# Performance work log

Hardware: AMD Instinct MI355X
Metric: run time of the kernel (lower is better)

Reference implementation:

```python
import jax, jax.numpy as jnp
import numpy as np
import math

B, C, H, W = 4, 128, 180, 180
CCAM, HEADS, DH, N = 256, 4, 32, 20000
HD = HEADS * DH
GAMMA = 0.08
EPS = 1e-6


def setup_inputs() -> dict:
    key = jax.random.key(0)
    ks = jax.random.split(key, 10)
    return {
        "lidar_bev": jax.random.normal(ks[0], (B, C, H, W), jnp.float32),
        "cam_bev_tokens": jax.random.normal(ks[1], (B, N, CCAM), jnp.float32),
        "gate_weights": jax.random.uniform(ks[2], (B, N), jnp.float32),
        "range_alpha": jax.random.uniform(ks[3], (1, 1, H, W), jnp.float32),
        # q_proj: Conv2d(C, HD, 1) -> weight [HD, C] (1x1 conv == per-pixel linear), bias [HD]
        "q_w": jax.random.normal(ks[4], (HD, C), jnp.float32) * 0.02,
        "q_bias": jax.random.normal(ks[5], (HD,), jnp.float32) * 0.02,
        # k/v_proj: Linear(CCAM, HD, bias=False)
        "k_w": jax.random.normal(ks[6], (HD, CCAM), jnp.float32) * 0.02,
        "v_w": jax.random.normal(ks[7], (HD, CCAM), jnp.float32) * 0.02,
        # out: Conv2d(HD, C, 1, bias=False) -> W_out [C, HD]
        "out_w": jax.random.normal(ks[8], (C, HD), jnp.float32) * 0.02,
        "cam_bev_indices": jax.random.randint(ks[9], (B, N, 2), 0, H, jnp.int32),
    }


def reference(lidar_bev, cam_bev_tokens, gate_weights, range_alpha,
              q_w, q_bias, k_w, v_w, out_w, cam_bev_indices):
    scale = 1.0 / math.sqrt(DH)
    # 1x1 conv q projection -> [B, h, d, H*W]
    q = jnp.einsum('bchw,oc->bohw', lidar_bev, q_w) + q_bias[None, :, None, None]
    q = q.reshape(B, HEADS, DH, H * W)

    i = jnp.clip(cam_bev_indices[..., 0], 0, H - 1)
    j = jnp.clip(cam_bev_indices[..., 1], 0, W - 1)
    lin = i * W + j  # [B, N]

    # gather q at sparse BEV locations -> [B, h, d, N]
    q_g = jnp.take_along_axis(q, lin[:, None, None, :], axis=3)

    # k/v projections -> [B, h, d, N]
    k = jnp.einsum('bnc,oc->bno', cam_bev_tokens, k_w).reshape(B, N, HEADS, DH).transpose(0, 2, 3, 1)
    v = jnp.einsum('bnc,oc->bno', cam_bev_tokens, v_w).reshape(B, N, HEADS, DH).transpose(0, 2, 3, 1)

    # elementwise-multiply attention: logits [B, h, N], softmax over the N tokens
    attn = jax.nn.softmax((q_g * k).sum(axis=2) * scale, axis=-1) * gate_weights[:, None, :]
    fused = (attn[:, :, None, :] * v).reshape(B, HD, N)  # [B, h*d, N]
    out_tok = jnp.einsum('co,bon->bcn', out_w, fused)    # [B, C, N]

    # per-batch scatter (index_add) + hit counts (bincount)
    def scatter_b(tok, lin_b):
        df = jnp.zeros((C, H * W), tok.dtype).at[:, lin_b].add(tok)
        hits = jnp.zeros((H * W,), tok.dtype).at[lin_b].add(1.0)
        return df, hits

    delta_flat, hits = jax.vmap(scatter_b)(out_tok, lin)  # [B,C,HW], [B,HW]
    mask = (hits > 0).astype(lidar_bev.dtype)  # [B, HW]

    # mean over hit locations (per batch, per channel), subtract on hits only
    mean_on = (delta_flat * mask[:, None, :]).sum(axis=-1, keepdims=True) \
              / (mask.sum(axis=-1)[:, None, None] + EPS)  # [B, C, 1]
    tmp = (delta_flat - mean_on * mask[:, None, :]).reshape(B, C, H, W)
    tmp = tmp * range_alpha * GAMMA
    return lidar_bev + tmp
```

## Files before the change

kernel.cpp:

```cpp
#include <hip/hip_runtime.h>

#define BB 4
#define CC 128
#define HH 180
#define WWW 180
#define HWHW (HH*WWW)
#define CCAMD 256
#define NHEADS 4
#define HDD 128
#define NT 20000
#define MTOT 80000
#define GAMMA_C 0.08f
#define EPS_C 1e-6f
#define SCALE_C 0.17677669529663687f

typedef short bf16x8 __attribute__((ext_vector_type(8)));
typedef float f32x4 __attribute__((ext_vector_type(4)));

typedef __attribute__((address_space(1))) const unsigned int GU;
typedef __attribute__((address_space(3))) unsigned int LU;

static __device__ __forceinline__ void gll16(const void* g, void* l) {
  __builtin_amdgcn_global_load_lds((GU*)g, (LU*)l, 16, 0, 0);
}

#define WAIT_VMCNT0() asm volatile("s_waitcnt vmcnt(0)" ::: "memory")
#define WAIT_VMCNT2() asm volatile("s_waitcnt vmcnt(2)" ::: "memory")
#define WAIT_VMCNT3() asm volatile("s_waitcnt vmcnt(3)" ::: "memory")
#define WAIT_LGKM0()  asm volatile("s_waitcnt lgkmcnt(0)" ::: "memory")

static __device__ __forceinline__ unsigned short f2bf(float x) {
  unsigned int b = __float_as_uint(x);
  unsigned int r = (b + 0x7fffu + ((b >> 16) & 1u)) >> 16;
  return (unsigned short)r;
}
static __device__ __forceinline__ float b2f(unsigned short u) {
  return __uint_as_float(((unsigned int)u) << 16);
}

static __device__ __forceinline__ float warpMax(float v) {
#pragma unroll
  for (int o = 32; o >= 1; o >>= 1) v = fmaxf(v, __shfl_xor(v, o));
  return v;
}
static __device__ __forceinline__ float warpSum(float v) {
#pragma unroll
  for (int o = 32; o >= 1; o >>= 1) v += __shfl_xor(v, o);
  return v;
}
static __device__ __forceinline__ int warpSumI(int v) {
#pragma unroll
  for (int o = 32; o >= 1; o >>= 1) v += __shfl_xor(v, o);
  return v;
}

__global__ __launch_bounds__(256) void k_prep_pix(
    const float* __restrict__ kw, const float* __restrict__ vw,
    const float* __restrict__ qw, const float* __restrict__ ow,
    unsigned short* __restrict__ kvw, unsigned short* __restrict__ qwb,
    unsigned short* __restrict__ owb, const int* __restrict__ cidx,
    int* __restrict__ pix_ws, int* __restrict__ cnt_pix)
{
  if (blockIdx.x < 96) {
    const int t = blockIdx.x * 256 + threadIdx.x;
    float4 f;
    unsigned short* dst;
    if (t < 16384) {
      f = (t < 8192) ? ((const float4*)kw)[t] : ((const float4*)vw)[t - 8192];
      dst = kvw + (size_t)t * 4;
    } else if (t < 20480) {
      const int i = t - 16384;
      f = ((const float4*)qw)[i];
      dst = qwb + (size_t)i * 4;
    } else {
      const int i = t - 20480;
      f = ((const float4*)ow)[i];
      dst = owb + (size_t)i * 4;
    }
    ushort4 u;
    u.x = f2bf(f.x); u.y = f2bf(f.y); u.z = f2bf(f.z); u.w = f2bf(f.w);
    *(ushort4*)dst = u;
  } else {
    const int t = (blockIdx.x - 96) * 256 + threadIdx.x;
    if (t >= MTOT) return;
    const int2 ij = *(const int2*)(cidx + (size_t)t * 2);
    int ii = ij.x; ii = ii < 0 ? 0 : (ii > HH - 1 ? HH - 1 : ii);
    int jj = ij.y; jj = jj < 0 ? 0 : (jj > WWW - 1 ? WWW - 1 : jj);
    const int pix = ii * WWW + jj;
    pix_ws[t] = pix;
    atomicAdd(cnt_pix + (size_t)(t / NT) * HWHW + pix, 1);
  }
}

template<int KSTEPS, int KW, int AMODE, int EPI, int NOUT>
static __device__ void pipe_body(
    int mblk, int nblk, unsigned short* lds,
    const float* __restrict__ Af32, const unsigned short* __restrict__ Abf,
    const unsigned short* __restrict__ Bw, const float* __restrict__ bias,
    unsigned short* __restrict__ Dbf, const int* __restrict__ pixw,
    float* __restrict__ aux, const unsigned short* __restrict__ kvb,
    float* __restrict__ meanr, const float* __restrict__ smMp,
    const float* __restrict__ smSinvp, const float* __restrict__ gatep,
    const float* __restrict__ logp, const int* __restrict__ sortn)
{
  const int tid = threadIdx.x;
  const int lane = tid & 63, wave = tid >> 6;
  const int wm = wave >> 2, wn = wave & 3;
  const int l16 = lane & 15, kg = lane >> 4;
  const int sr_rd = (l16 >> 1) & 3;

  const int row_s = wave * 16 + (lane >> 2);
  const int chunk_s = lane & 3;
  const int swz_s = chunk_s ^ ((lane >> 3) & 3);
  const int a_dst = row_s * 32 + swz_s * 8;

  const unsigned short* bsrc = Bw + (size_t)(nblk * 128 + row_s) * KW + swz_s * 8;

  const float* asrc_f32 = nullptr;
  const unsigned short* asrc_bf = nullptr;
  float coef4[4] = {0.f, 0.f, 0.f, 0.f};
  if constexpr (AMODE == 0) {
    asrc_f32 = Af32 + (size_t)(mblk * 128 + row_s) * KW + chunk_s * 8;
  } else if constexpr (AMODE == 2) {
    const int r = mblk * 128 + row_s;
    const int bb = r / NT;
    asrc_bf = Abf + ((size_t)bb * HWHW + pixw[r]) * 128 + swz_s * 8;
  } else {
    const int r = mblk * 128 + row_s;
    const int bb = r / NT, pos = r - bb * NT;
    const int n = sortn[(size_t)bb * NT + pos];
    asrc_bf = Abf + ((size_t)bb * NT + n) * 256 + 128 + chunk_s * 8;
    const float ga = gatep[(size_t)bb * NT + n];
#pragma unroll
    for (int h = 0; h < 4; ++h) {
      const int bh = bb * NHEADS + h;
      coef4[h] = __expf(logp[(size_t)bh * NT + n] - smMp[bh]) * smSinvp[bh] * ga;
    }
  }

  f32x4 acc[4][2];
#pragma unroll
  for (int i = 0; i < 4; ++i)
#pragma unroll
    for (int j = 0; j < 2; ++j) acc[i][j] = (f32x4)0.0f;

  float4 afx[2], afy[2];
  bf16x8 av[2];

  auto issueA = [&](int kt, int s, int buf) {
    if constexpr (AMODE == 0) {
      afx[s] = *(const float4*)(asrc_f32 + kt * 32);
      afy[s] = *(const float4*)(asrc_f32 + kt * 32 + 4);
    } else if constexpr (AMODE == 2) {
      gll16(asrc_bf + kt * 32, &lds[buf * 8192 + wave * 512]);
    } else {
      av[s] = *(const bf16x8*)(asrc_bf + kt * 32);
    }
  };
  auto issueB = [&](int kt, int buf) {
    gll16(bsrc + kt * 32, &lds[buf * 8192 + 4096 + wave * 512]);
  };
  auto writeA = [&](int kt, int s, int buf) {
    bf16x8 v;
    if constexpr (AMODE == 0) {
      v[0] = (short)f2bf(afx[s].x); v[1] = (short)f2bf(afx[s].y);
      v[2] = (short)f2bf(afx[s].z); v[3] = (short)f2bf(afx[s].w);
      v[4] = (short)f2bf(afy[s].x); v[5] = (short)f2bf(afy[s].y);
      v[6] = (short)f2bf(afy[s].z); v[7] = (short)f2bf(afy[s].w);
    } else {
      const float c = coef4[kt];
#pragma unroll
      for (int e = 0; e < 8; ++e)
        v[e] = (short)f2bf(b2f((unsigned short)av[s][e]) * c);
    }
    *(bf16x8*)&lds[buf * 8192 + a_dst] = v;
  };
  auto compute = [&](int buf) {
    const int base = buf * 8192;
    bf16x8 a[4], b[2];
#pragma unroll
    for (int mf = 0; mf < 4; ++mf) {
      const int row = wm * 64 + mf * 16 + l16;
      a[mf] = *(const bf16x8*)&lds[base + row * 32 + ((kg ^ sr_rd) << 3)];
    }
#pragma unroll
    for (int nf = 0; nf < 2; ++nf) {
      const int row = wn * 32 + nf * 16 + l16;
      b[nf] = *(const bf16x8*)&lds[base + 4096 + row * 32 + ((kg ^ sr_rd) << 3)];
    }
#pragma unroll
    for (int mf = 0; mf < 4; ++mf)
#pragma unroll
      for (int nf = 0; nf < 2; ++nf)
        acc[mf][nf] =
            __builtin_amdgcn_mfma_f32_16x16x32_bf16(a[mf], b[nf], acc[mf][nf], 0, 0, 0);
  };

  issueA(0, 0, 0); issueB(0, 0);
  issueA(1, 1, 1); issueB(1, 1);
  if constexpr (AMODE != 2) writeA(0, 0, 0);

#pragma unroll
  for (int t = 0; t < KSTEPS; ++t) {
    if (t < KSTEPS - 1) {
      if constexpr (AMODE == 0) WAIT_VMCNT3(); else WAIT_VMCNT2();
    } else {
      WAIT_VMCNT0();
    }
    WAIT_LGKM0();
    __builtin_amdgcn_s_barrier();
    __builtin_amdgcn_sched_barrier(0);
    if (t + 2 < KSTEPS) {
      issueA(t + 2, t & 1, (t + 2) % 3);
      issueB(t + 2, (t + 2) % 3);
    }
    compute(t % 3);
    if constexpr (AMODE != 2) {
      if (t + 1 < KSTEPS) writeA(t + 1, (t + 1) & 1, (t + 1) % 3);
    }
  }
  __syncthreads();

  float* scratch = (float*)lds;

  if constexpr (EPI == 0) {
#pragma unroll
    for (int mf = 0; mf < 4; ++mf) {
#pragma unroll
      for (int j = 0; j < 4; ++j) {
        const int row = mblk * 128 + wm * 64 + mf * 16 + kg * 4 + j;
        unsigned short* dr = Dbf + (size_t)row * NOUT + nblk * 128 + wn * 32 + l16;
#pragma unroll
        for (int nf = 0; nf < 2; ++nf)
          dr[nf * 16] = f2bf(acc[mf][nf][j]);
      }
    }
  } else if constexpr (EPI == 2) {
    float bv[2];
#pragma unroll
    for (int nf = 0; nf < 2; ++nf)
      bv[nf] = bias[wn * 32 + nf * 16 + l16];
#pragma unroll
    for (int mf = 0; mf < 4; ++mf) {
#pragma unroll
      for (int j = 0; j < 4; ++j) {
        const int rl = wm * 64 + mf * 16 + kg * 4 + j;
        const int row = mblk * 128 + rl;
        const unsigned short* kr = kvb + (size_t)row * 256 + wn * 32 + l16;
        float s = (acc[mf][0][j] + bv[0]) * b2f(kr[0]) +
                  (acc[mf][1][j] + bv[1]) * b2f(kr[16]);
        s += __shfl_xor(s, 8, 16); s += __shfl_xor(s, 4, 16);
        s += __shfl_xor(s, 2, 16); s += __shfl_xor(s, 1, 16);
        if (l16 == 0) scratch[rl * 4 + wn] = s;
      }
    }
    __syncthreads();
    if (tid < 128) {
      const int row = mblk * 128 + tid;
      const int bb = row / NT, n = row - bb * NT;
#pragma unroll
      for (int h = 0; h < 4; ++h)
        aux[((size_t)bb * NHEADS + h) * NT + n] = scratch[tid * 4 + h] * SCALE_C;
    }
  } else {
    if (tid < 256) scratch[tid] = 0.0f;
    __syncthreads();
    const int b0 = (mblk * 128) / NT;
#pragma unroll
    for (int mf = 0; mf < 4; ++mf) {
      const int baser = mblk * 128 + wm * 64 + mf * 16 + kg * 4;
      const int bb = baser / NT;
      const int bsel = (bb != b0) ? 1 : 0;
      float s[2] = {0.0f, 0.0f};
#pragma unroll
      for (int j = 0; j < 4; ++j) {
        const int row = baser + j;
        unsigned short* dr = Dbf + (size_t)row * 128 + wn * 32 + l16;
#pragma unroll
        for (int nf = 0; nf < 2; ++nf) {
          dr[nf * 16] = f2bf(acc[mf][nf][j]);
          s[nf] += acc[mf][nf][j];
        }
      }
#pragma unroll
      for (int nf = 0; nf < 2; ++nf)
        atomicAdd(&scratch[bsel * 128 + wn * 32 + nf * 16 + l16], s[nf]);
    }
    __syncthreads();
    const int b1 = (mblk * 128 + 127) / NT;
    if (tid < 128) atomicAdd(meanr + (size_t)b0 * 128 + tid, scratch[tid]);
    else if (tid < 256 && b1 != b0)
      atomicAdd(meanr + (size_t)b1 * 128 + (tid - 128), scratch[tid]);
  }
}

__global__ __launch_bounds__(512) void k_m1(
    const float* __restrict__ lidar, unsigned short* __restrict__ lidar_t,
    const int* __restrict__ cnt_pix, int* __restrict__ bsum,
    const float* __restrict__ tokens, const unsigned short* __restrict__ kvw,
    unsigned short* __restrict__ kv_bf)
{
  __shared__ unsigned short lds[24576];
  const int bid = blockIdx.x;
  if (bid < 254) {
    const int idx = bid * 512 + threadIdx.x;
    if (idx >= BB * HWHW) return;
    const int b = idx / HWHW, p = idx - b * HWHW;
    const float* src = lidar + (size_t)b * CC * HWHW + p;
    unsigned short* dst = lidar_t + (size_t)idx * 128;
#pragma unroll
    for (int c8 = 0; c8 < 16; ++c8) {
      bf16x8 v;
#pragma unroll
      for (int e = 0; e < 8; ++e)
        v[e] = (short)f2bf(src[(size_t)(c8 * 8 + e) * HWHW]);
      ((bf16x8*)dst)[c8] = v;
    }
  } else if (bid < 510) {
    __shared__ int ws[8];
    const int s = bid - 254;
    const int b = s >> 6, blk = s & 63;
    const int idx = blk * 512 + threadIdx.x;
    int v = (idx < HWHW) ? cnt_pix[(size_t)b * HWHW + idx] : 0;
    v = warpSumI(v);
    const int wave = threadIdx.x >> 6, lane = threadIdx.x & 63;
    if (lane == 0) ws[wave] = v;
    __syncthreads();
    if (threadIdx.x == 0) {
      int s8 = 0;
#pragma unroll
      for (int w = 0; w < 8; ++w) s8 += ws[w];
      bsum[b * 64 + blk] = s8;
    }
  } else {
    const int g = bid - 510;
    pipe_body<8, 256, 0, 0, 256>(g % 625, g / 625, lds, tokens, nullptr,
                                 kvw, nullptr, kv_bf, nullptr, nullptr,
                                 nullptr, nullptr, nullptr, nullptr,
                                 nullptr, nullptr, nullptr);
  }
}

__global__ __launch_bounds__(64) void k_scanB(
    const int* __restrict__ bsum, int* __restrict__ boff)
{
  const int b = blockIdx.x, t = threadIdx.x;
  const int v = bsum[b * 64 + t];
  int inc = v;
#pragma unroll
  for (int off = 1; off < 64; off <<= 1) {
    int u = __shfl_up(inc, off, 64);
    if (t >= off) inc += u;
  }
  boff[b * 64 + t] = inc - v;
}

__global__ __launch_bounds__(512) void k_m2(
    const int* __restrict__ cnt_pix, const int* __restrict__ boff,
    int* __restrict__ start, const unsigned short* __restrict__ lidar_t,
    const unsigned short* __restrict__ qwb, const float* __restrict__ qb,
    const int* __restrict__ pixw, float* __restrict__ logits,
    const unsigned short* __restrict__ kv_bf)
{
  __shared__ unsigned short lds[24576];
  const int bid = blockIdx.x;
  if (bid < 256) {
    __shared__ int ws[8];
    const int b = bid >> 6, blk = bid & 63;
    const int idx = blk * 512 + threadIdx.x;
    const int wave = threadIdx.x >> 6, lane = threadIdx.x & 63;
    int v = (idx < HWHW) ? cnt_pix[(size_t)b * HWHW + idx] : 0;
    int inc = v;
#pragma unroll
    for (int off = 1; off < 64; off <<= 1) {
      int u = __shfl_up(inc, off, 64);
      if (lane >= off) inc += u;
    }
    if (lane == 63) ws[wave] = inc;
    __syncthreads();
    int wo = 0;
#pragma unroll
    for (int w = 0; w < 8; ++w)
      if (w < wave) wo += ws[w];
    if (idx < HWHW)
      start[(size_t)b * HWHW + idx] = boff[b * 64 + blk] + wo + inc - v;
  } else {
    pipe_body<4, 128, 2, 2, 128>(bid - 256, 0, lds, nullptr, lidar_t, qwb,
                                 qb, nullptr, pixw, logits, kv_bf, nullptr,
                                 nullptr, nullptr, nullptr, nullptr, nullptr);
  }
}

__global__ __launch_bounds__(256) void k_m3(
    const float* __restrict__ logits, float* __restrict__ pm,
    float* __restrict__ ps, const int* __restrict__ pix_ws,
    const int* __restrict__ start, int* __restrict__ fill,
    int* __restrict__ sortn)
{
  const int bid = blockIdx.x;
  if (bid < 128) {
    const int ch = bid & 7, bh = bid >> 3;
    const float* L = logits + (size_t)bh * NT + ch * 2500;
    const int tid = threadIdx.x;
    __shared__ float sred[4];

    float m = -INFINITY;
    for (int i = tid; i < 2500; i += 256) m = fmaxf(m, L[i]);
    m = warpMax(m);
    if ((tid & 63) == 0) sred[tid >> 6] = m;
    __syncthreads();
    m = fmaxf(fmaxf(sred[0], sred[1]), fmaxf(sred[2], sred[3]));

    float s = 0.0f;
    for (int i = tid; i < 2500; i += 256) s += __expf(L[i] - m);
    s = warpSum(s);
    __syncthreads();
    if ((tid & 63) == 0) sred[tid >> 6] = s;
    __syncthreads();
    if (tid == 0) {
      pm[bh * 8 + ch] = m;
      ps[bh * 8 + ch] = sred[0] + sred[1] + sred[2] + sred[3];
    }
  } else {
    const int t = (bid - 128) * 256 + threadIdx.x;
    if (t >= MTOT) return;
    const int b = t / NT, n = t - b * NT;
    const int pix = pix_ws[t];
    const int pos = atomicAdd(fill + (size_t)b * HWHW + pix, 1);
    sortn[(size_t)b * NT + start[(size_t)b * HWHW + pix] + pos] = n;
  }
}

__global__ __launch_bounds__(256) void k_cntfix(
    const int* __restrict__ cnt_pix, float* __restrict__ cntB,
    const float* __restrict__ pm, const float* __restrict__ ps,
    float* __restrict__ smM, float* __restrict__ smSinv)
{
  const int b = blockIdx.x;
  const int tid = threadIdx.x;
  float s = 0.0f;
  for (int i = tid; i < HWHW; i += 256)
    s += (cnt_pix[(size_t)b * HWHW + i] > 0) ? 1.0f : 0.0f;
  s = warpSum(s);
  __shared__ float sred[4];
  if ((tid & 63) == 0) sred[tid >> 6] = s;
  __syncthreads();
  if (tid == 0) cntB[b] = sred[0] + sred[1] + sred[2] + sred[3];
  if (b == 0 && tid < BB * NHEADS) {
    float M = -INFINITY;
#pragma unroll
    for (int c = 0; c < 8; ++c) M = fmaxf(M, pm[tid * 8 + c]);
    float S = 0.0f;
#pragma unroll
    for (int c = 0; c < 8; ++c) S += ps[tid * 8 + c] * __expf(pm[tid * 8 + c] - M);
    smM[tid] = M;
    smSinv[tid] = 1.0f / S;
  }
}

__global__ __launch_bounds__(512) void k_out(
    const unsigned short* __restrict__ kv_bf, const unsigned short* __restrict__ owb,
    unsigned short* __restrict__ out_tok, float* __restrict__ meanr,
    const float* __restrict__ smM, const float* __restrict__ smSinv,
    const float* __restrict__ gate, const float* __restrict__ logits,
    const int* __restrict__ sortn)
{
  __shared__ unsigned short lds[24576];
  pipe_body<4, 128, 4, 3, 128>(blockIdx.x, 0, lds, nullptr, kv_bf, owb,
                               nullptr, out_tok, nullptr, nullptr, nullptr,
                               meanr, smM, smSinv, gate, logits, sortn);
}

__global__ __launch_bounds__(512) void k_final2(
    const float* __restrict__ lidar, const float* __restrict__ alpha,
    const int* __restrict__ cnt_pix, const int* __restrict__ start,
    const unsigned short* __restrict__ out_tok,
    const float* __restrict__ mean_raw, const float* __restrict__ cntB,
    float* __restrict__ out)
{
  __shared__ float tile[80 * 136];
  const int b = blockIdx.y;
  const int p0 = blockIdx.x * 80;
  const int t = threadIdx.x;

  const int g = t >> 5, l32 = t & 31;
#pragma unroll
  for (int i = 0; i < 5; ++i) {
    const int pl = i * 16 + g;
    const int p = p0 + pl;
    const int st = start[(size_t)b * HWHW + p];
    const int cn = cnt_pix[(size_t)b * HWHW + p];
    float4 a = make_float4(0.0f, 0.0f, 0.0f, 0.0f);
    const unsigned short* rp = out_tok + ((size_t)b * NT + st) * 128 + l32 * 4;
    for (int k = 0; k < cn; ++k) {
      const ushort4 u = *(const ushort4*)(rp + (size_t)k * 128);
      a.x += b2f(u.x); a.y += b2f(u.y); a.z += b2f(u.z); a.w += b2f(u.w);
    }
    *(float4*)&tile[pl * 136 + ((l32 ^ (pl & 7)) << 2)] = a;
  }
  __syncthreads();

  const int c = t >> 2, sub = t & 3;
  const int cq = c >> 2, cr = c & 3;
  const float mn = mean_raw[b * 128 + c] / (cntB[b] + EPS_C);
  const size_t cbase = ((size_t)b * CC + c) * HWHW + p0;
  const int* cnb = cnt_pix + (size_t)b * HWHW + p0;
#pragma unroll
  for (int j = 0; j < 5; ++j) {
    const int pq = j * 16 + sub * 4;
    float4 d;
    d.x = tile[(pq + 0) * 136 + (((cq ^ ((pq + 0) & 7)) << 2) | cr)];
    d.y = tile[(pq + 1) * 136 + (((cq ^ ((pq + 1) & 7)) << 2) | cr)];
    d.z = tile[(pq + 2) * 136 + (((cq ^ ((pq + 2) & 7)) << 2) | cr)];
    d.w = tile[(pq + 3) * 136 + (((cq ^ ((pq + 3) & 7)) << 2) | cr)];
    const float4 li = *(const float4*)(lidar + cbase + pq);
    const float4 al = *(const float4*)(alpha + p0 + pq);
    const int4 hc = *(const int4*)(cnb + pq);
    float4 o;
    o.x = li.x + (d.x - (hc.x > 0 ? mn : 0.0f)) * al.x * GAMMA_C;
    o.y = li.y + (d.y - (hc.y > 0 ? mn : 0.0f)) * al.y * GAMMA_C;
    o.z = li.z + (d.z - (hc.z > 0 ? mn : 0.0f)) * al.z * GAMMA_C;
    o.w = li.w + (d.w - (hc.w > 0 ? mn : 0.0f)) * al.w * GAMMA_C;
    *(float4*)(out + cbase + pq) = o;
  }
}

extern "C" void kernel_launch(void* const* d_in, const int* in_sizes, int n_in,
                              void* d_out, int out_size, void* d_ws, size_t ws_size,
                              hipStream_t stream)
{
  const float* lidar  = (const float*)d_in[0];
  const float* tokens = (const float*)d_in[1];
  const float* gate   = (const float*)d_in[2];
  const float* alpha  = (const float*)d_in[3];
  const float* q_w    = (const float*)d_in[4];
  const float* q_b    = (const float*)d_in[5];
  const float* k_w    = (const float*)d_in[6];
  const float* v_w    = (const float*)d_in[7];
  const float* out_w  = (const float*)d_in[8];
  const int*   cidx   = (const int*)d_in[9];
  float* out = (float*)d_out;

  char* W = (char*)d_ws;
  unsigned short* kv_bf   = (unsigned short*)(W + 0);
  unsigned short* lidar_t = (unsigned short*)(W + 40960000);
  unsigned short* out_tok = (unsigned short*)(W + 74137600);
  float* logits  = (float*)(W + 94617600);
  int*   pix_ws  = (int*)(W + 95897600);
  int*   sortn   = (int*)(W + 96217600);
  int*   cnt_pix = (int*)(W + 96537600);
  int*   start   = (int*)(W + 97056000);
  int*   fill    = (int*)(W + 97574400);
  float* mean_raw = (float*)(W + 98092800);
  float* cntB     = (float*)(W + 98094848);
  unsigned short* kvw_bf = (unsigned short*)(W + 98094912);
  unsigned short* qw_bf  = (unsigned short*)(W + 98225984);
  unsigned short* ow_bf  = (unsigned short*)(W + 98258752);
  float* pm     = (float*)(W + 98291520);
  float* ps     = (float*)(W + 98292032);
  float* smM    = (float*)(W + 98292544);
  float* smSinv = (float*)(W + 98292608);
  int*   bsum   = (int*)(W + 98292672);
  int*   boff   = (int*)(W + 98293696);

  hipMemsetAsync(cnt_pix, 0, (size_t)BB * HWHW * sizeof(int), stream);
  hipMemsetAsync(fill, 0, (size_t)BB * HWHW * sizeof(int), stream);
  hipMemsetAsync(mean_raw, 0, 2048 + 64, stream);

  k_prep_pix<<<dim3(409), 256, 0, stream>>>(k_w, v_w, q_w, out_w, kvw_bf,
                                            qw_bf, ow_bf, cidx, pix_ws, cnt_pix);
  k_m1<<<dim3(1760), 512, 0, stream>>>(lidar, lidar_t, cnt_pix, bsum,
                                       tokens, kvw_bf, kv_bf);
  k_scanB<<<dim3(BB), 64, 0, stream>>>(bsum, boff);
  k_m2<<<dim3(881), 512, 0, stream>>>(cnt_pix, boff, start, lidar_t, qw_bf,
                                      q_b, pix_ws, logits, kv_bf);
  k_m3<<<dim3(441), 256, 0, stream>>>(logits, pm, ps, pix_ws, start, fill, sortn);
  k_cntfix<<<dim3(BB), 256, 0, stream>>>(cnt_pix, cntB, pm, ps, smM, smSinv);
  k_out<<<dim3(625), 512, 0, stream>>>(kv_bf, ow_bf, out_tok, mean_raw,
                                       smM, smSinv, gate, logits, sortn);
  k_final2<<<dim3(405, BB), 512, 0, stream>>>(lidar, alpha, cnt_pix, start,
                                              out_tok, mean_raw, cntB, out);
}
```

Baseline: 208.4 us.

## Split fused k_m1 into separate kernels and move hit-count into scan pass

Splits the heterogeneous k_m1 launch (transpose, block sums, KV GEMM) into three separate kernels: k_tr2b, k_scanA and k_kv. The per-batch hit-count reduction moves from the 4-block k_cntfix serial loop into k_scanA, which accumulates the count with a float atomicAdd. The softmax fixup becomes a single tiny kernel. This removes the slow 4-block reduction over the count array and gives each kernel a uniform block shape, at the cost of two extra launches and less overlap between the transpose and the GEMM.

```diff
diff --git a/kernel.cpp b/kernel.cpp
--- a/kernel.cpp
+++ b/kernel.cpp
@@ -92,6 +92,61 @@
   }
 }
 
+__global__ __launch_bounds__(512) void k_tr2b(
+    const float* __restrict__ lidar, unsigned short* __restrict__ lidar_t)
+{
+  const int idx = blockIdx.x * 512 + threadIdx.x;
+  if (idx >= BB * HWHW) return;
+  const int b = idx / HWHW, p = idx - b * HWHW;
+  const float* src = lidar + (size_t)b * CC * HWHW + p;
+  unsigned short* dst = lidar_t + (size_t)idx * 128;
+#pragma unroll
+  for (int c8 = 0; c8 < 16; ++c8) {
+    bf16x8 v;
+#pragma unroll
+    for (int e = 0; e < 8; ++e)
+      v[e] = (short)f2bf(src[(size_t)(c8 * 8 + e) * HWHW]);
+    ((bf16x8*)dst)[c8] = v;
+  }
+}
+
+__global__ __launch_bounds__(512) void k_scanA(
+    const int* __restrict__ cnt, int* __restrict__ bsum,
+    float* __restrict__ cntB)
+{
+  const int b = blockIdx.y, blk = blockIdx.x;
+  const int idx = blk * 512 + threadIdx.x;
+  int v = (idx < HWHW) ? cnt[(size_t)b * HWHW + idx] : 0;
+  int h = (v > 0) ? 1 : 0;
+  v = warpSumI(v);
+  h = warpSumI(h);
+  __shared__ int ws[8], hs[8];
+  const int wave = threadIdx.x >> 6, lane = threadIdx.x & 63;
+  if (lane == 0) { ws[wave] = v; hs[wave] = h; }
+  __syncthreads();
+  if (threadIdx.x == 0) {
+    int sv = 0, sh = 0;
+#pragma unroll
+    for (int w = 0; w < 8; ++w) { sv += ws[w]; sh += hs[w]; }
+    bsum[b * 64 + blk] = sv;
+    atomicAdd(cntB + b, (float)sh);
+  }
+}
+
+__global__ __launch_bounds__(64) void k_scanB(
+    const int* __restrict__ bsum, int* __restrict__ boff)
+{
+  const int b = blockIdx.x, t = threadIdx.x;
+  const int v = bsum[b * 64 + t];
+  int inc = v;
+#pragma unroll
+  for (int off = 1; off < 64; off <<= 1) {
+    int u = __shfl_up(inc, off, 64);
+    if (t >= off) inc += u;
+  }
+  boff[b * 64 + t] = inc - v;
+}
+
 template<int KSTEPS, int KW, int AMODE, int EPI, int NOUT>
 static __device__ void pipe_body(
     int mblk, int nblk, unsigned short* lds,
@@ -294,65 +349,15 @@
   }
 }
 
-__global__ __launch_bounds__(512) void k_m1(
-    const float* __restrict__ lidar, unsigned short* __restrict__ lidar_t,
-    const int* __restrict__ cnt_pix, int* __restrict__ bsum,
+__global__ __launch_bounds__(512) void k_kv(
     const float* __restrict__ tokens, const unsigned short* __restrict__ kvw,
     unsigned short* __restrict__ kv_bf)
 {
   __shared__ unsigned short lds[24576];
-  const int bid = blockIdx.x;
-  if (bid < 254) {
-    const int idx = bid * 512 + threadIdx.x;
-    if (idx >= BB * HWHW) return;
-    const int b = idx / HWHW, p = idx - b * HWHW;
-    const float* src = lidar + (size_t)b * CC * HWHW + p;
-    unsigned short* dst = lidar_t + (size_t)idx * 128;
-#pragma unroll
-    for (int c8 = 0; c8 < 16; ++c8) {
-      bf16x8 v;
-#pragma unroll
-      for (int e = 0; e < 8; ++e)
-        v[e] = (short)f2bf(src[(size_t)(c8 * 8 + e) * HWHW]);
-      ((bf16x8*)dst)[c8] = v;
-    }
-  } else if (bid < 510) {
-    __shared__ int ws[8];
-    const int s = bid - 254;
-    const int b = s >> 6, blk = s & 63;
-    const int idx = blk * 512 + threadIdx.x;
-    int v = (idx < HWHW) ? cnt_pix[(size_t)b * HWHW + idx] : 0;
-    v = warpSumI(v);
-    const int wave = threadIdx.x >> 6, lane = threadIdx.x & 63;
-    if (lane == 0) ws[wave] = v;
-    __syncthreads();
-    if (threadIdx.x == 0) {
-      int s8 = 0;
-#pragma unroll
-      for (int w = 0; w < 8; ++w) s8 += ws[w];
-      bsum[b * 64 + blk] = s8;
-    }
-  } else {
-    const int g = bid - 510;
-    pipe_body<8, 256, 0, 0, 256>(g % 625, g / 625, lds, tokens, nullptr,
-                                 kvw, nullptr, kv_bf, nullptr, nullptr,
-                                 nullptr, nullptr, nullptr, nullptr,
-                                 nullptr, nullptr, nullptr);
-  }
-}
-
-__global__ __launch_bounds__(64) void k_scanB(
-    const int* __restrict__ bsum, int* __restrict__ boff)
-{
-  const int b = blockIdx.x, t = threadIdx.x;
-  const int v = bsum[b * 64 + t];
-  int inc = v;
-#pragma unroll
-  for (int off = 1; off < 64; off <<= 1) {
-    int u = __shfl_up(inc, off, 64);
-    if (t >= off) inc += u;
-  }
-  boff[b * 64 + t] = inc - v;
+  pipe_body<8, 256, 0, 0, 256>(blockIdx.x, blockIdx.y, lds, tokens, nullptr,
+                               kvw, nullptr, kv_bf, nullptr, nullptr,
+                               nullptr, nullptr, nullptr, nullptr,
+                               nullptr, nullptr, nullptr);
 }
 
 __global__ __launch_bounds__(512) void k_m2(
@@ -431,31 +436,20 @@
   }
 }
 
-__global__ __launch_bounds__(256) void k_cntfix(
-    const int* __restrict__ cnt_pix, float* __restrict__ cntB,
+__global__ __launch_bounds__(64) void k_smfix(
     const float* __restrict__ pm, const float* __restrict__ ps,
     float* __restrict__ smM, float* __restrict__ smSinv)
 {
-  const int b = blockIdx.x;
-  const int tid = threadIdx.x;
-  float s = 0.0f;
-  for (int i = tid; i < HWHW; i += 256)
-    s += (cnt_pix[(size_t)b * HWHW + i] > 0) ? 1.0f : 0.0f;
-  s = warpSum(s);
-  __shared__ float sred[4];
-  if ((tid & 63) == 0) sred[tid >> 6] = s;
-  __syncthreads();
-  if (tid == 0) cntB[b] = sred[0] + sred[1] + sred[2] + sred[3];
-  if (b == 0 && tid < BB * NHEADS) {
-    float M = -INFINITY;
-#pragma unroll
-    for (int c = 0; c < 8; ++c) M = fmaxf(M, pm[tid * 8 + c]);
-    float S = 0.0f;
-#pragma unroll
-    for (int c = 0; c < 8; ++c) S += ps[tid * 8 + c] * __expf(pm[tid * 8 + c] - M);
-    smM[tid] = M;
-    smSinv[tid] = 1.0f / S;
-  }
+  const int t = threadIdx.x;
+  if (t >= BB * NHEADS) return;
+  float M = -INFINITY;
+#pragma unroll
+  for (int c = 0; c < 8; ++c) M = fmaxf(M, pm[t * 8 + c]);
+  float S = 0.0f;
+#pragma unroll
+  for (int c = 0; c < 8; ++c) S += ps[t * 8 + c] * __expf(pm[t * 8 + c] - M);
+  smM[t] = M;
+  smSinv[t] = 1.0f / S;
 }
 
 __global__ __launch_bounds__(512) void k_out(
@@ -569,13 +563,14 @@
 
   k_prep_pix<<<dim3(409), 256, 0, stream>>>(k_w, v_w, q_w, out_w, kvw_bf,
                                             qw_bf, ow_bf, cidx, pix_ws, cnt_pix);
-  k_m1<<<dim3(1760), 512, 0, stream>>>(lidar, lidar_t, cnt_pix, bsum,
-                                       tokens, kvw_bf, kv_bf);
+  k_tr2b<<<dim3(254), 512, 0, stream>>>(lidar, lidar_t);
+  k_scanA<<<dim3(64, BB), 512, 0, stream>>>(cnt_pix, bsum, cntB);
   k_scanB<<<dim3(BB), 64, 0, stream>>>(bsum, boff);
+  k_kv<<<dim3(625, 2), 512, 0, stream>>>(tokens, kvw_bf, kv_bf);
   k_m2<<<dim3(881), 512, 0, stream>>>(cnt_pix, boff, start, lidar_t, qw_bf,
                                       q_b, pix_ws, logits, kv_bf);
   k_m3<<<dim3(441), 256, 0, stream>>>(logits, pm, ps, pix_ws, start, fill, sortn);
-  k_cntfix<<<dim3(BB), 256, 0, stream>>>(cnt_pix, cntB, pm, ps, smM, smSinv);
+  k_smfix<<<dim3(1), 64, 0, stream>>>(pm, ps, smM, smSinv);
   k_out<<<dim3(625), 512, 0, stream>>>(kv_bf, ow_bf, out_tok, mean_raw,
                                        smM, smSinv, gate, logits, sortn);
   k_final2<<<dim3(405, BB), 512, 0, stream>>>(lidar, alpha, cnt_pix, start,
```

Result: faster. 184.7 us (median of 2 runs) (-11.4%).
